# Optimization experiments

Hardware: AMD Instinct MI355X
Metric: run time of the kernel (lower is better)

Reference implementation:

```python
import jax, jax.numpy as jnp
import numpy as np

N, F_IN, H, O = 4096, 512, 4, 256
ALPHA = 0.2  # leaky-relu negative slope
NEG = -9e15  # mask value for non-edges (matches DAEGC)


def setup_inputs() -> dict:
    key = jax.random.key(0)
    ks = jax.random.split(key, 9)
    x = jax.random.normal(ks[0], (N, F_IN), jnp.float32)
    adj = (jax.random.uniform(ks[1], (N, N)) < 0.01).astype(jnp.float32)
    adj = jnp.maximum(adj, jnp.eye(N, dtype=jnp.float32))
    M = jax.random.uniform(ks[2], (N, N), dtype=jnp.float32)  # proximity matrix
    s0 = 1.0 / np.sqrt(F_IN)
    s1 = 1.0 / np.sqrt(H * O)
    W0 = jax.random.normal(ks[3], (H, F_IN, O), jnp.float32) * s0
    a_self0 = jax.random.normal(ks[4], (H, O), jnp.float32) * 0.1
    a_neigh0 = jax.random.normal(ks[5], (H, O), jnp.float32) * 0.1
    W1 = jax.random.normal(ks[6], (H, H * O, O), jnp.float32) * s1
    a_self1 = jax.random.normal(ks[7], (H, O), jnp.float32) * 0.1
    a_neigh1 = jax.random.normal(ks[8], (H, O), jnp.float32) * 0.1
    return dict(x=x, adj=adj, M=M, W0=W0, a_self0=a_self0, a_neigh0=a_neigh0,
                W1=W1, a_self1=a_self1, a_neigh1=a_neigh1)


def gat_layer(x, adj, M, W, a_s, a_n, concat):
    # x: [N, F_in], W: [H, F_in, O]
    h = jnp.einsum('nf,hfo->hno', x, W)                      # [H, N, O]
    e = (jnp.einsum('hno,ho->hn', h, a_s)[:, :, None]
         + jnp.einsum('hno,ho->hn', h, a_n)[:, None, :])     # [H, N, N]
    e = jax.nn.leaky_relu(e * M[None], ALPHA)
    e = jnp.where(adj[None] > 0, e, NEG)
    attn = jax.nn.softmax(e, axis=-1)                        # masked neighbor softmax
    out = jnp.einsum('hnm,hmo->hno', attn, h)                # [H, N, O]
    if concat:
        return jax.nn.elu(out.transpose(1, 0, 2).reshape(x.shape[0], -1))  # [N, H*O]
    return out.mean(axis=0)                                  # [N, O]


def reference(x, adj, M, W0, a_self0, a_neigh0, W1, a_self1, a_neigh1):
    h = gat_layer(x, adj, M, W0, a_self0, a_neigh0, True)
    h = gat_layer(h, adj, M, W1, a_self1, a_neigh1, False)
    # F.normalize(h, p=2, dim=1) with eps=1e-12
    z = h / jnp.maximum(jnp.linalg.norm(h, axis=1, keepdims=True), 1e-12)
    A_pred = jax.nn.sigmoid(z @ z.T)                          # dot-product decode [N, N]
    return (A_pred, z)
```

## Files before the change

kernel.cpp:

```cpp
#include <hip/hip_runtime.h>
#include <hip/hip_bf16.h>
#include <math.h>

#define N_NODES 4096
#define F_IN0   512
#define HEADS   4
#define O_DIM   256
#define HO      1024
#define LRELU_A 0.2f
#define MAXE    192
#define LOG2E   1.44269504088896f

typedef __bf16 bf16_t;
typedef bf16_t bf16x8 __attribute__((ext_vector_type(8)));
typedef float f32x4 __attribute__((ext_vector_type(4)));
typedef unsigned short u16x8 __attribute__((ext_vector_type(8)));

__device__ __forceinline__ unsigned short f2b(float f) {
    __hip_bfloat16 t = __float2bfloat16(f);
    return __builtin_bit_cast(unsigned short, t);
}
__device__ __forceinline__ float b2f(unsigned short u) {
    unsigned int v = ((unsigned int)u) << 16;
    return __builtin_bit_cast(float, v);
}
__device__ __forceinline__ float fexp(float x) {
    return __builtin_amdgcn_exp2f(x * LOG2E);
}
__device__ __forceinline__ float fsigmoid(float x) {
    return __builtin_amdgcn_rcpf(1.f + __builtin_amdgcn_exp2f(-x * LOG2E));
}

#define GLOAD_LDS(g, l) \
    __builtin_amdgcn_global_load_lds((const __attribute__((address_space(1))) unsigned int*)(g), \
                                     (__attribute__((address_space(3))) unsigned int*)(l), 16, 0, 0)

__device__ __forceinline__ void transpose_tile(const float* __restrict__ W,
                                               unsigned short* __restrict__ Wt,
                                               int K, int O, int kt, int ot, int h,
                                               float (*t)[33], int tid) {
    const float* Wh = W + (size_t)h * K * O;
    unsigned short* Wth = Wt + (size_t)h * K * O;
    const int k0 = kt * 32, o0 = ot * 32;
    const int tx = tid & 31, ty = tid >> 5;
    for (int r = ty; r < 32; r += 8) t[r][tx] = Wh[(size_t)(k0 + r) * O + o0 + tx];
    __syncthreads();
    for (int r = ty; r < 32; r += 8)
        Wth[(size_t)(o0 + r) * K + k0 + tx] = f2b(t[tx][r]);
}

__global__ __launch_bounds__(256) void conv_k(const float* __restrict__ x,
                                              const float* __restrict__ W0,
                                              const float* __restrict__ W1,
                                              unsigned short* __restrict__ xb,
                                              unsigned short* __restrict__ wt0,
                                              unsigned short* __restrict__ wt1) {
    __shared__ float t[32][33];
    const int b = blockIdx.x;
    const int tid = threadIdx.x;
    if (b < 2048) {
        int i = b * 256 + tid;
        float4 v = ((const float4*)x)[i];
        ushort4 o;
        o.x = f2b(v.x); o.y = f2b(v.y); o.z = f2b(v.z); o.w = f2b(v.w);
        ((ushort4*)xb)[i] = o;
    } else if (b < 2560) {
        int b2 = b - 2048;
        transpose_tile(W0, wt0, F_IN0, O_DIM, (b2 & 15), ((b2 >> 4) & 7), b2 >> 7, t, tid);
    } else {
        int b2 = b - 2560;
        transpose_tile(W1, wt1, HO, O_DIM, (b2 & 31), ((b2 >> 5) & 7), b2 >> 8, t, tid);
    }
}

__global__ __launch_bounds__(256) void edge_k(const float* __restrict__ adj,
                                              int* __restrict__ ecnt,
                                              int* __restrict__ eidx) {
    const int w    = threadIdx.x >> 6;
    const int lane = threadIdx.x & 63;
    const int n    = blockIdx.x * 4 + w;
    const float* adjr = adj + (size_t)n * N_NODES;
    float4 a4[16];
#pragma unroll
    for (int it = 0; it < 16; ++it)
        a4[it] = *(const float4*)&adjr[lane * 4 + it * 256];
    unsigned long long mask = 0;
#pragma unroll
    for (int it = 0; it < 16; ++it) {
        if (a4[it].x > 0.f) mask |= 1ull << (it * 4 + 0);
        if (a4[it].y > 0.f) mask |= 1ull << (it * 4 + 1);
        if (a4[it].z > 0.f) mask |= 1ull << (it * 4 + 2);
        if (a4[it].w > 0.f) mask |= 1ull << (it * 4 + 3);
    }
    const int ec = __popcll(mask);
    int sc = ec;
#pragma unroll
    for (int off = 1; off < 64; off <<= 1) {
        int u = __shfl_up(sc, off, 64);
        if (lane >= off) sc += u;
    }
    int base = sc - ec;
    unsigned long long mm = mask;
    while (mm) {
        const int q = __builtin_ctzll(mm);
        mm &= mm - 1;
        const int m = lane * 4 + ((q >> 2) << 8) + (q & 3);
        eidx[(size_t)n * MAXE + base] = m;
        ++base;
    }
    if (lane == 63) ecnt[n] = sc;
}

__global__ __launch_bounds__(256) void mfma_nt(const bf16_t* __restrict__ A,
                                               const bf16_t* __restrict__ B,
                                               unsigned short* __restrict__ Cv,
                                               int K, int ldc,
                                               unsigned long long bStride,
                                               unsigned long long cStride) {
    B += blockIdx.z * bStride;
    const size_t zoff = (size_t)blockIdx.z * cStride;
    __shared__ bf16_t sAB[2][2][64 * 32];
    const int tid  = threadIdx.x;
    const int lane = tid & 63;
    const int wave = tid >> 6;
    const int wr = (wave >> 1) * 32;
    const int wc = (wave & 1) * 32;
    const int rowBase = blockIdx.x * 64;
    const int colBase = blockIdx.y * 64;
    const int l15  = lane & 15;
    const int quad = lane >> 4;

    const int sm = tid & 63;
    const int sc = tid >> 6;
    const bf16_t* aRow = A + (size_t)(rowBase + sm) * K + sc * 8;
    const bf16_t* bRow = B + (size_t)(colBase + sm) * K + sc * 8;

    f32x4 acc[2][2] = {};

    GLOAD_LDS(aRow, &sAB[0][0][tid * 8]);
    GLOAD_LDS(bRow, &sAB[0][1][tid * 8]);
    __syncthreads();

    int cur = 0;
    for (int k0 = 0; k0 < K; k0 += 32) {
        if (k0 + 32 < K) {
            GLOAD_LDS(aRow + k0 + 32, &sAB[cur ^ 1][0][tid * 8]);
            GLOAD_LDS(bRow + k0 + 32, &sAB[cur ^ 1][1][tid * 8]);
        }
        bf16x8 af[2], bfr[2];
#pragma unroll
        for (int i = 0; i < 2; ++i) {
            af[i]  = *(bf16x8*)&sAB[cur][0][(quad * 64 + wr + i * 16 + l15) * 8];
            bfr[i] = *(bf16x8*)&sAB[cur][1][(quad * 64 + wc + i * 16 + l15) * 8];
        }
#pragma unroll
        for (int i = 0; i < 2; ++i)
#pragma unroll
            for (int j = 0; j < 2; ++j)
                acc[i][j] = __builtin_amdgcn_mfma_f32_16x16x32_bf16(af[i], bfr[j], acc[i][j], 0, 0, 0);
        __syncthreads();
        cur ^= 1;
    }

    const int orow = rowBase + wr + quad * 4;
    const int ocol = colBase + wc + l15;
#pragma unroll
    for (int i = 0; i < 2; ++i)
#pragma unroll
        for (int j = 0; j < 2; ++j)
#pragma unroll
            for (int r = 0; r < 4; ++r)
                Cv[zoff + (size_t)(orow + i * 16 + r) * ldc + ocol + j * 16] = f2b(acc[i][j][r]);
}

#define EP_STRIDE 132
__global__ __launch_bounds__(256) void decode_k(const bf16_t* __restrict__ Z,
                                                float* __restrict__ out) {
    __shared__ float smem_f[8192];
    bf16_t* base = (bf16_t*)smem_f;
    float*  sE = smem_f;

    const int tid  = threadIdx.x;
    const int lane = tid & 63;
    const int wave = tid >> 6;
    const int wr = (wave >> 1) * 64;
    const int wc = (wave & 1) * 64;
    const int rowBase = blockIdx.x * 128;
    const int colBase = blockIdx.y * 128;
    const int l15  = lane & 15;
    const int quad = lane >> 4;

    const int sm = tid & 127;
    const int sc = tid >> 7;
    const bf16_t* aRow = Z + (size_t)(rowBase + sm) * O_DIM + sc * 8;
    const bf16_t* bRow = Z + (size_t)(colBase + sm) * O_DIM + sc * 8;

    f32x4 acc[4][4] = {};

    GLOAD_LDS(aRow,      base + tid * 8);
    GLOAD_LDS(aRow + 16, base + (256 + tid) * 8);
    GLOAD_LDS(bRow,      base + 4096 + tid * 8);
    GLOAD_LDS(bRow + 16, base + 4096 + (256 + tid) * 8);
    __syncthreads();

    int cur = 0;
    for (int k0 = 0; k0 < O_DIM; k0 += 32) {
        if (k0 + 32 < O_DIM) {
            bf16_t* nA = base + (cur ^ 1) * 8192;
            GLOAD_LDS(aRow + k0 + 32, nA + tid * 8);
            GLOAD_LDS(aRow + k0 + 48, nA + (256 + tid) * 8);
            GLOAD_LDS(bRow + k0 + 32, nA + 4096 + tid * 8);
            GLOAD_LDS(bRow + k0 + 48, nA + 4096 + (256 + tid) * 8);
        }
        bf16_t* sA = base + cur * 8192;
        bf16_t* sB = sA + 4096;
        bf16x8 af[4], bfr[4];
#pragma unroll
        for (int i = 0; i < 4; ++i) {
            af[i]  = *(bf16x8*)&sA[(quad * 128 + wr + i * 16 + l15) * 8];
            bfr[i] = *(bf16x8*)&sB[(quad * 128 + wc + i * 16 + l15) * 8];
        }
#pragma unroll
        for (int i = 0; i < 4; ++i)
#pragma unroll
            for (int j = 0; j < 4; ++j)
                acc[i][j] = __builtin_amdgcn_mfma_f32_16x16x32_bf16(af[i], bfr[j], acc[i][j], 0, 0, 0);
        __syncthreads();
        cur ^= 1;
    }

    const int lrBase = (wave >> 1) * 16;
    for (int i = 0; i < 4; ++i) {
#pragma unroll
        for (int j = 0; j < 4; ++j)
#pragma unroll
            for (int r = 0; r < 4; ++r)
                sE[(lrBase + quad * 4 + r) * EP_STRIDE + wc + j * 16 + l15] = acc[i][j][r];
        __syncthreads();
#pragma unroll
        for (int p = 0; p < 4; ++p) {
            const int idx4 = p * 256 + tid;
            const int lr = idx4 >> 5;
            const int c4 = idx4 & 31;
            f32x4 v = *(f32x4*)&sE[lr * EP_STRIDE + c4 * 4];
            f32x4 o;
            o[0] = fsigmoid(v[0]); o[1] = fsigmoid(v[1]);
            o[2] = fsigmoid(v[2]); o[3] = fsigmoid(v[3]);
            const int grow = rowBase + (lr >> 4) * 64 + i * 16 + (lr & 15);
            *(f32x4*)&out[(size_t)grow * N_NODES + colBase + c4 * 4] = o;
        }
        __syncthreads();
    }
}

__global__ __launch_bounds__(256) void scores_k(const unsigned short* __restrict__ hb,
                                                const float* __restrict__ a_s,
                                                const float* __restrict__ a_n,
                                                float* __restrict__ s_self4,
                                                float* __restrict__ s_neigh4) {
    const int n = blockIdx.x;
    const int head = threadIdx.x >> 6;
    const int lane = threadIdx.x & 63;
    const ushort4 hv = *(const ushort4*)&hb[(size_t)n * HO + head * O_DIM + lane * 4];
    const float4 av = *(const float4*)&a_s[head * O_DIM + lane * 4];
    const float4 nv = *(const float4*)&a_n[head * O_DIM + lane * 4];
    float h0 = b2f(hv.x), h1 = b2f(hv.y), h2 = b2f(hv.z), h3 = b2f(hv.w);
    float ps = h0 * av.x + h1 * av.y + h2 * av.z + h3 * av.w;
    float pn = h0 * nv.x + h1 * nv.y + h2 * nv.z + h3 * nv.w;
    for (int off = 32; off; off >>= 1) {
        ps += __shfl_down(ps, off, 64);
        pn += __shfl_down(pn, off, 64);
    }
    if (lane == 0) {
        s_self4[n * HEADS + head]  = ps;
        s_neigh4[n * HEADS + head] = pn;
    }
}

__global__ __launch_bounds__(256) void attn_k(const unsigned short* __restrict__ hb,
                                              const int* __restrict__ ecnt,
                                              const int* __restrict__ eidx,
                                              const float* __restrict__ Mm,
                                              const float* __restrict__ s_self4,
                                              const float* __restrict__ s_neigh4,
                                              unsigned short* __restrict__ out0,
                                              float* __restrict__ out1, int layer) {
    const int n = blockIdx.x;
    const int tid = threadIdx.x;
    __shared__ int midx[MAXE];
    __shared__ float ev[MAXE][HEADS];
    __shared__ float red2[2][HO];
    const int c = ecnt[n];

    if (tid < c) {
        const int m = eidx[(size_t)n * MAXE + tid];
        const float Mv = Mm[((size_t)n << 12) + m];
        midx[tid] = m;
        const float4 ss = *(const float4*)&s_self4[n * HEADS];
        const float4 sn = *(const float4*)&s_neigh4[m * HEADS];
        float e0 = (ss.x + sn.x) * Mv, e1 = (ss.y + sn.y) * Mv;
        float e2 = (ss.z + sn.z) * Mv, e3 = (ss.w + sn.w) * Mv;
        ev[tid][0] = e0 > 0.f ? e0 : LRELU_A * e0;
        ev[tid][1] = e1 > 0.f ? e1 : LRELU_A * e1;
        ev[tid][2] = e2 > 0.f ? e2 : LRELU_A * e2;
        ev[tid][3] = e3 > 0.f ? e3 : LRELU_A * e3;
    }
    __syncthreads();

    {
        const int w = tid >> 6, lane = tid & 63;
        float mx = -1e30f;
        for (int k = lane; k < c; k += 64) mx = fmaxf(mx, ev[k][w]);
        for (int off = 32; off; off >>= 1) mx = fmaxf(mx, __shfl_xor(mx, off, 64));
        float s = 0.f;
        for (int k = lane; k < c; k += 64) {
            float p = fexp(ev[k][w] - mx);
            ev[k][w] = p;
            s += p;
        }
        for (int off = 32; off; off >>= 1) s += __shfl_xor(s, off, 64);
        float inv = __builtin_amdgcn_rcpf(s);
        for (int k = lane; k < c; k += 64) ev[k][w] *= inv;
    }
    __syncthreads();

    const int half = tid >> 7;
    const int t    = tid & 127;
    const int hh   = t >> 5;
    float acc[8] = {};
#pragma unroll 2
    for (int k = half; k < c; k += 2) {
        const int m = midx[k];
        const float w = ev[k][hh];
        const u16x8 hv = *(const u16x8*)&hb[(size_t)m * HO + t * 8];
#pragma unroll
        for (int j = 0; j < 8; ++j) acc[j] += w * b2f(hv[j]);
    }
#pragma unroll
    for (int j = 0; j < 8; ++j) red2[half][t * 8 + j] = acc[j];
    __syncthreads();

    if (layer == 0) {
        const int o = tid * 4;
        ushort4 ov;
        float v0 = red2[0][o + 0] + red2[1][o + 0];
        float v1 = red2[0][o + 1] + red2[1][o + 1];
        float v2 = red2[0][o + 2] + red2[1][o + 2];
        float v3 = red2[0][o + 3] + red2[1][o + 3];
        ov.x = f2b(v0 > 0.f ? v0 : fexp(v0) - 1.f);
        ov.y = f2b(v1 > 0.f ? v1 : fexp(v1) - 1.f);
        ov.z = f2b(v2 > 0.f ? v2 : fexp(v2) - 1.f);
        ov.w = f2b(v3 > 0.f ? v3 : fexp(v3) - 1.f);
        *(ushort4*)&out0[(size_t)n * HO + o] = ov;
    } else {
        const int o = tid;
        float v = 0.f;
#pragma unroll
        for (int h = 0; h < HEADS; ++h)
            v += red2[0][h * O_DIM + o] + red2[1][h * O_DIM + o];
        out1[(size_t)n * O_DIM + o] = 0.25f * v;
    }
}

__global__ __launch_bounds__(256) void norm_k(float* __restrict__ z,
                                              unsigned short* __restrict__ zb) {
    const int n = blockIdx.x;
    const int tid = threadIdx.x;
    float v = z[(size_t)n * O_DIM + tid];
    float p = v * v;
    for (int off = 32; off; off >>= 1) p += __shfl_down(p, off, 64);
    __shared__ float wsum[4];
    if ((tid & 63) == 0) wsum[tid >> 6] = p;
    __syncthreads();
    float ssq = wsum[0] + wsum[1] + wsum[2] + wsum[3];
    float denom = fmaxf(sqrtf(ssq), 1e-12f);
    float zn = v / denom;
    z[(size_t)n * O_DIM + tid] = zn;
    zb[(size_t)n * O_DIM + tid] = f2b(zn);
}

extern "C" void kernel_launch(void* const* d_in, const int* in_sizes, int n_in,
                              void* d_out, int out_size, void* d_ws, size_t ws_size,
                              hipStream_t stream) {
    const float* x   = (const float*)d_in[0];
    const float* adj = (const float*)d_in[1];
    const float* Mm  = (const float*)d_in[2];
    const float* W0  = (const float*)d_in[3];
    const float* as0 = (const float*)d_in[4];
    const float* an0 = (const float*)d_in[5];
    const float* W1  = (const float*)d_in[6];
    const float* as1 = (const float*)d_in[7];
    const float* an1 = (const float*)d_in[8];
    float* out = (float*)d_out;

    unsigned short* hb    = (unsigned short*)d_ws;
    unsigned short* hin1b = hb + (size_t)N_NODES * HO;
    unsigned short* xb    = hin1b + (size_t)N_NODES * HO;
    unsigned short* wt0   = xb + (size_t)N_NODES * F_IN0;
    unsigned short* wt1   = wt0 + HEADS * O_DIM * F_IN0;
    unsigned short* zb    = wt1 + HEADS * O_DIM * HO;
    float* s_self4  = (float*)(zb + (size_t)N_NODES * O_DIM);
    float* s_neigh4 = s_self4 + N_NODES * HEADS;
    int*   eidx = (int*)(s_neigh4 + N_NODES * HEADS);
    int*   ecnt = eidx + (size_t)N_NODES * MAXE;
    float* zbuf = out + (size_t)N_NODES * N_NODES;

    conv_k<<<3584, 256, 0, stream>>>(x, W0, W1, xb, wt0, wt1);
    edge_k<<<1024, 256, 0, stream>>>(adj, ecnt, eidx);

    mfma_nt<<<dim3(64, 4, 4), 256, 0, stream>>>((const bf16_t*)xb, (const bf16_t*)wt0, hb,
                                                F_IN0, HO,
                                                (unsigned long long)O_DIM * F_IN0,
                                                (unsigned long long)O_DIM);
    scores_k<<<N_NODES, 256, 0, stream>>>(hb, as0, an0, s_self4, s_neigh4);
    attn_k<<<N_NODES, 256, 0, stream>>>(hb, ecnt, eidx, Mm, s_self4, s_neigh4, hin1b, nullptr, 0);

    mfma_nt<<<dim3(64, 4, 4), 256, 0, stream>>>((const bf16_t*)hin1b, (const bf16_t*)wt1, hb,
                                                HO, HO,
                                                (unsigned long long)O_DIM * HO,
                                                (unsigned long long)O_DIM);
    scores_k<<<N_NODES, 256, 0, stream>>>(hb, as1, an1, s_self4, s_neigh4);
    attn_k<<<N_NODES, 256, 0, stream>>>(hb, ecnt, eidx, Mm, s_self4, s_neigh4, nullptr, zbuf, 1);

    norm_k<<<N_NODES, 256, 0, stream>>>(zbuf, zb);
    decode_k<<<dim3(32, 32), 256, 0, stream>>>((const bf16_t*)zb, out);
}
```

Measured before the change: 324.3 us.

## Fuse edge extraction into prep, attention scores into GEMM epilogue, norm into attn

Merges the edge-list kernel into the conversion/transpose prep kernel, which also zeroes the score accumulators. Computes the per-node self/neighbor attention scores inside the MFMA GEMM epilogue using shuffle reductions and atomicAdd, removing the separate scores kernels. Folds the L2 normalization into the layer-1 attention kernel. This cuts four launches and a reread of h, at the cost of atomics and of scores computed from fp32 accumulators instead of bf16-rounded h.

```diff
diff --git a/kernel.cpp b/kernel.cpp
--- a/kernel.cpp
+++ b/kernel.cpp
@@ -49,12 +49,16 @@
         Wth[(size_t)(o0 + r) * K + k0 + tx] = f2b(t[tx][r]);
 }
 
-__global__ __launch_bounds__(256) void conv_k(const float* __restrict__ x,
+__global__ __launch_bounds__(256) void prep_k(const float* __restrict__ x,
                                               const float* __restrict__ W0,
                                               const float* __restrict__ W1,
+                                              const float* __restrict__ adj,
                                               unsigned short* __restrict__ xb,
                                               unsigned short* __restrict__ wt0,
-                                              unsigned short* __restrict__ wt1) {
+                                              unsigned short* __restrict__ wt1,
+                                              int* __restrict__ ecnt,
+                                              int* __restrict__ eidx,
+                                              float* __restrict__ szero) {
     __shared__ float t[32][33];
     const int b = blockIdx.x;
     const int tid = threadIdx.x;
@@ -67,53 +71,54 @@
     } else if (b < 2560) {
         int b2 = b - 2048;
         transpose_tile(W0, wt0, F_IN0, O_DIM, (b2 & 15), ((b2 >> 4) & 7), b2 >> 7, t, tid);
-    } else {
+    } else if (b < 3584) {
         int b2 = b - 2560;
         transpose_tile(W1, wt1, HO, O_DIM, (b2 & 31), ((b2 >> 5) & 7), b2 >> 8, t, tid);
-    }
-}
-
-__global__ __launch_bounds__(256) void edge_k(const float* __restrict__ adj,
-                                              int* __restrict__ ecnt,
-                                              int* __restrict__ eidx) {
-    const int w    = threadIdx.x >> 6;
-    const int lane = threadIdx.x & 63;
-    const int n    = blockIdx.x * 4 + w;
-    const float* adjr = adj + (size_t)n * N_NODES;
-    float4 a4[16];
-#pragma unroll
-    for (int it = 0; it < 16; ++it)
-        a4[it] = *(const float4*)&adjr[lane * 4 + it * 256];
-    unsigned long long mask = 0;
-#pragma unroll
-    for (int it = 0; it < 16; ++it) {
-        if (a4[it].x > 0.f) mask |= 1ull << (it * 4 + 0);
-        if (a4[it].y > 0.f) mask |= 1ull << (it * 4 + 1);
-        if (a4[it].z > 0.f) mask |= 1ull << (it * 4 + 2);
-        if (a4[it].w > 0.f) mask |= 1ull << (it * 4 + 3);
-    }
-    const int ec = __popcll(mask);
-    int sc = ec;
-#pragma unroll
-    for (int off = 1; off < 64; off <<= 1) {
-        int u = __shfl_up(sc, off, 64);
-        if (lane >= off) sc += u;
-    }
-    int base = sc - ec;
-    unsigned long long mm = mask;
-    while (mm) {
-        const int q = __builtin_ctzll(mm);
-        mm &= mm - 1;
-        const int m = lane * 4 + ((q >> 2) << 8) + (q & 3);
-        eidx[(size_t)n * MAXE + base] = m;
-        ++base;
-    }
-    if (lane == 63) ecnt[n] = sc;
+    } else {
+        const int w    = tid >> 6;
+        const int lane = tid & 63;
+        const int n    = (b - 3584) * 4 + w;
+        const float* adjr = adj + (size_t)n * N_NODES;
+        float4 a4[16];
+#pragma unroll
+        for (int it = 0; it < 16; ++it)
+            a4[it] = *(const float4*)&adjr[lane * 4 + it * 256];
+        unsigned long long mask = 0;
+#pragma unroll
+        for (int it = 0; it < 16; ++it) {
+            if (a4[it].x > 0.f) mask |= 1ull << (it * 4 + 0);
+            if (a4[it].y > 0.f) mask |= 1ull << (it * 4 + 1);
+            if (a4[it].z > 0.f) mask |= 1ull << (it * 4 + 2);
+            if (a4[it].w > 0.f) mask |= 1ull << (it * 4 + 3);
+        }
+        const int ec = __popcll(mask);
+        int sc = ec;
+#pragma unroll
+        for (int off = 1; off < 64; off <<= 1) {
+            int u = __shfl_up(sc, off, 64);
+            if (lane >= off) sc += u;
+        }
+        int base = sc - ec;
+        unsigned long long mm = mask;
+        while (mm) {
+            const int q = __builtin_ctzll(mm);
+            mm &= mm - 1;
+            const int m = lane * 4 + ((q >> 2) << 8) + (q & 3);
+            eidx[(size_t)n * MAXE + base] = m;
+            ++base;
+        }
+        if (lane == 63) ecnt[n] = sc;
+        if (lane < 16) szero[(size_t)(lane >> 2) * N_NODES * HEADS + n * HEADS + (lane & 3)] = 0.f;
+    }
 }
 
 __global__ __launch_bounds__(256) void mfma_nt(const bf16_t* __restrict__ A,
                                                const bf16_t* __restrict__ B,
                                                unsigned short* __restrict__ Cv,
+                                               const float* __restrict__ a_s,
+                                               const float* __restrict__ a_n,
+                                               float* __restrict__ s_self,
+                                               float* __restrict__ s_neigh,
                                                int K, int ldc,
                                                unsigned long long bStride,
                                                unsigned long long cStride) {
@@ -171,6 +176,39 @@
 #pragma unroll
             for (int r = 0; r < 4; ++r)
                 Cv[zoff + (size_t)(orow + i * 16 + r) * ldc + ocol + j * 16] = f2b(acc[i][j][r]);
+
+    float ps[2][4] = {}, pn[2][4] = {};
+#pragma unroll
+    for (int j = 0; j < 2; ++j) {
+        const float av = a_s[blockIdx.z * O_DIM + ocol + j * 16];
+        const float nv = a_n[blockIdx.z * O_DIM + ocol + j * 16];
+#pragma unroll
+        for (int i = 0; i < 2; ++i)
+#pragma unroll
+            for (int r = 0; r < 4; ++r) {
+                ps[i][r] += acc[i][j][r] * av;
+                pn[i][r] += acc[i][j][r] * nv;
+            }
+    }
+#pragma unroll
+    for (int off = 1; off < 16; off <<= 1)
+#pragma unroll
+        for (int i = 0; i < 2; ++i)
+#pragma unroll
+            for (int r = 0; r < 4; ++r) {
+                ps[i][r] += __shfl_xor(ps[i][r], off, 64);
+                pn[i][r] += __shfl_xor(pn[i][r], off, 64);
+            }
+    if (l15 == 0) {
+#pragma unroll
+        for (int i = 0; i < 2; ++i)
+#pragma unroll
+            for (int r = 0; r < 4; ++r) {
+                const int row = orow + i * 16 + r;
+                atomicAdd(&s_self[row * HEADS + blockIdx.z],  ps[i][r]);
+                atomicAdd(&s_neigh[row * HEADS + blockIdx.z], pn[i][r]);
+            }
+    }
 }
 
 #define EP_STRIDE 132
@@ -253,30 +291,6 @@
     }
 }
 
-__global__ __launch_bounds__(256) void scores_k(const unsigned short* __restrict__ hb,
-                                                const float* __restrict__ a_s,
-                                                const float* __restrict__ a_n,
-                                                float* __restrict__ s_self4,
-                                                float* __restrict__ s_neigh4) {
-    const int n = blockIdx.x;
-    const int head = threadIdx.x >> 6;
-    const int lane = threadIdx.x & 63;
-    const ushort4 hv = *(const ushort4*)&hb[(size_t)n * HO + head * O_DIM + lane * 4];
-    const float4 av = *(const float4*)&a_s[head * O_DIM + lane * 4];
-    const float4 nv = *(const float4*)&a_n[head * O_DIM + lane * 4];
-    float h0 = b2f(hv.x), h1 = b2f(hv.y), h2 = b2f(hv.z), h3 = b2f(hv.w);
-    float ps = h0 * av.x + h1 * av.y + h2 * av.z + h3 * av.w;
-    float pn = h0 * nv.x + h1 * nv.y + h2 * nv.z + h3 * nv.w;
-    for (int off = 32; off; off >>= 1) {
-        ps += __shfl_down(ps, off, 64);
-        pn += __shfl_down(pn, off, 64);
-    }
-    if (lane == 0) {
-        s_self4[n * HEADS + head]  = ps;
-        s_neigh4[n * HEADS + head] = pn;
-    }
-}
-
 __global__ __launch_bounds__(256) void attn_k(const unsigned short* __restrict__ hb,
                                               const int* __restrict__ ecnt,
                                               const int* __restrict__ eidx,
@@ -284,12 +298,15 @@
                                               const float* __restrict__ s_self4,
                                               const float* __restrict__ s_neigh4,
                                               unsigned short* __restrict__ out0,
-                                              float* __restrict__ out1, int layer) {
+                                              float* __restrict__ out1,
+                                              unsigned short* __restrict__ zb,
+                                              int layer) {
     const int n = blockIdx.x;
     const int tid = threadIdx.x;
     __shared__ int midx[MAXE];
     __shared__ float ev[MAXE][HEADS];
     __shared__ float red2[2][HO];
+    __shared__ float ws2[4];
     const int c = ecnt[n];
 
     if (tid < c) {
@@ -358,25 +375,17 @@
 #pragma unroll
         for (int h = 0; h < HEADS; ++h)
             v += red2[0][h * O_DIM + o] + red2[1][h * O_DIM + o];
-        out1[(size_t)n * O_DIM + o] = 0.25f * v;
-    }
-}
-
-__global__ __launch_bounds__(256) void norm_k(float* __restrict__ z,
-                                              unsigned short* __restrict__ zb) {
-    const int n = blockIdx.x;
-    const int tid = threadIdx.x;
-    float v = z[(size_t)n * O_DIM + tid];
-    float p = v * v;
-    for (int off = 32; off; off >>= 1) p += __shfl_down(p, off, 64);
-    __shared__ float wsum[4];
-    if ((tid & 63) == 0) wsum[tid >> 6] = p;
-    __syncthreads();
-    float ssq = wsum[0] + wsum[1] + wsum[2] + wsum[3];
-    float denom = fmaxf(sqrtf(ssq), 1e-12f);
-    float zn = v / denom;
-    z[(size_t)n * O_DIM + tid] = zn;
-    zb[(size_t)n * O_DIM + tid] = f2b(zn);
+        v *= 0.25f;
+        float p = v * v;
+        for (int off = 32; off; off >>= 1) p += __shfl_down(p, off, 64);
+        if ((tid & 63) == 0) ws2[tid >> 6] = p;
+        __syncthreads();
+        const float ssq = ws2[0] + ws2[1] + ws2[2] + ws2[3];
+        const float denom = fmaxf(sqrtf(ssq), 1e-12f);
+        const float zn = v / denom;
+        out1[(size_t)n * O_DIM + o] = zn;
+        zb[(size_t)n * O_DIM + o]   = f2b(zn);
+    }
 }
 
 extern "C" void kernel_launch(void* const* d_in, const int* in_sizes, int n_in,
@@ -399,29 +408,29 @@
     unsigned short* wt0   = xb + (size_t)N_NODES * F_IN0;
     unsigned short* wt1   = wt0 + HEADS * O_DIM * F_IN0;
     unsigned short* zb    = wt1 + HEADS * O_DIM * HO;
-    float* s_self4  = (float*)(zb + (size_t)N_NODES * O_DIM);
-    float* s_neigh4 = s_self4 + N_NODES * HEADS;
-    int*   eidx = (int*)(s_neigh4 + N_NODES * HEADS);
+    float* s0s = (float*)(zb + (size_t)N_NODES * O_DIM);
+    float* s0n = s0s + (size_t)N_NODES * HEADS;
+    float* s1s = s0n + (size_t)N_NODES * HEADS;
+    float* s1n = s1s + (size_t)N_NODES * HEADS;
+    int*   eidx = (int*)(s1n + (size_t)N_NODES * HEADS);
     int*   ecnt = eidx + (size_t)N_NODES * MAXE;
     float* zbuf = out + (size_t)N_NODES * N_NODES;
 
-    conv_k<<<3584, 256, 0, stream>>>(x, W0, W1, xb, wt0, wt1);
-    edge_k<<<1024, 256, 0, stream>>>(adj, ecnt, eidx);
+    prep_k<<<4608, 256, 0, stream>>>(x, W0, W1, adj, xb, wt0, wt1, ecnt, eidx, s0s);
 
     mfma_nt<<<dim3(64, 4, 4), 256, 0, stream>>>((const bf16_t*)xb, (const bf16_t*)wt0, hb,
+                                                as0, an0, s0s, s0n,
                                                 F_IN0, HO,
                                                 (unsigned long long)O_DIM * F_IN0,
                                                 (unsigned long long)O_DIM);
-    scores_k<<<N_NODES, 256, 0, stream>>>(hb, as0, an0, s_self4, s_neigh4);
-    attn_k<<<N_NODES, 256, 0, stream>>>(hb, ecnt, eidx, Mm, s_self4, s_neigh4, hin1b, nullptr, 0);
+    attn_k<<<N_NODES, 256, 0, stream>>>(hb, ecnt, eidx, Mm, s0s, s0n, hin1b, nullptr, nullptr, 0);
 
     mfma_nt<<<dim3(64, 4, 4), 256, 0, stream>>>((const bf16_t*)hin1b, (const bf16_t*)wt1, hb,
+                                                as1, an1, s1s, s1n,
                                                 HO, HO,
                                                 (unsigned long long)O_DIM * HO,
                                                 (unsigned long long)O_DIM);
-    scores_k<<<N_NODES, 256, 0, stream>>>(hb, as1, an1, s_self4, s_neigh4);
-    attn_k<<<N_NODES, 256, 0, stream>>>(hb, ecnt, eidx, Mm, s_self4, s_neigh4, nullptr, zbuf, 1);
-
-    norm_k<<<N_NODES, 256, 0, stream>>>(zbuf, zb);
+    attn_k<<<N_NODES, 256, 0, stream>>>(hb, ecnt, eidx, Mm, s1s, s1n, nullptr, zbuf, zb, 1);
+
     decode_k<<<dim3(32, 32), 256, 0, stream>>>((const bf16_t*)zb, out);
 }
```

Result: slower. 338.2 us (+4.3%).
